# Kernel optimization log

Hardware: AMD Instinct MI355X
Metric: run time of the kernel (lower is better)

The kernel has to match this reference:

```python
import jax, jax.numpy as jnp
import numpy as np

N_DOF = 7
WIDTH = 1024
BATCH = 8192
EPS = 1e-5
LSIZE = N_DOF * (N_DOF + 1) // 2   # diag (n) + strictly-lower ((n^2-n)/2)


def _tri_idx(n):
    # order matches LowTri: offset -i chunks, within-chunk j -> entry (j+i, j)
    r, c = [], []
    for i in range(n):
        for j in range(n - i):
            r.append(j + i)
            c.append(j)
    return np.array(r, np.int32), np.array(c, np.int32)

_R, _C = _tri_idx(N_DOF)


def setup_inputs() -> dict:
    key = jax.random.key(0)
    ks = jax.random.split(key, 9)

    def glorot(k, shape):
        std = (2.0 / (shape[0] + shape[1])) ** 0.5
        return (jax.random.normal(k, shape, jnp.float32) * std).astype(jnp.float32)

    lower = LSIZE - N_DOF
    b0 = 0.1
    return {
        "state": jax.random.normal(ks[0], (BATCH, N_DOF), jnp.float32),
        "velocity": jax.random.normal(ks[1], (BATCH, N_DOF), jnp.float32),
        "acceleration": jax.random.normal(ks[2], (BATCH, N_DOF), jnp.float32),
        "W_in": glorot(ks[3], (N_DOF, WIDTH)), "b_in": jnp.full((WIDTH,), b0, jnp.float32),
        "W_h": glorot(ks[4], (WIDTH, WIDTH)), "b_h": jnp.full((WIDTH,), b0, jnp.float32),
        "W_g": glorot(ks[5], (WIDTH, 1)), "b_g": jnp.full((1,), b0, jnp.float32),
        "W_ld": glorot(ks[6], (WIDTH, N_DOF)), "b_ld": jnp.full((N_DOF,), b0, jnp.float32),
        "W_lo": glorot(ks[7], (WIDTH, lower)), "b_lo": jnp.full((lower,), b0, jnp.float32),
    }


def _layer(x, der, W, b, act):
    # a: [B, out]; der: [B, in, n_dof] -> [B, out, n_dof]
    a = x @ W + b
    if act == "relu":
        y = jax.nn.relu(a)
        gp = (a > 0).astype(a.dtype)
    else:  # linear
        y = a
        gp = jnp.ones_like(a)
    # diag(g'(a)) @ W^T @ prev_der  ==  g'(a)[:, :, None] * (W^T @ prev_der)
    new_der = gp[:, :, None] * jnp.einsum("io,bid->bod", W, der)
    return y, new_der


def _forward(state, velocity, acceleration,
             W_in, b_in, W_h, b_h, W_g, b_g, W_ld, b_ld, W_lo, b_lo):
    B = state.shape[0]
    eye = jnp.broadcast_to(jnp.eye(N_DOF, dtype=state.dtype), (B, N_DOF, N_DOF))

    y1, d1 = _layer(state, eye, W_in, b_in, "relu")
    y2, d2 = _layer(y1, d1, W_h, b_h, "relu")
    y3, d3 = _layer(y2, d2, W_h, b_h, "relu")   # original reuses hidden_layer1 twice

    V, derV = _layer(y3, d3, W_g, b_g, "linear")       # derV: [B, 1, n_dof]
    l_diag, der_ld = _layer(y3, d3, W_ld, b_ld, "relu")
    l_low, der_lo = _layer(y3, d3, W_lo, b_lo, "linear")

    l = jnp.concatenate([l_diag, l_low], axis=1)          # [B, LSIZE]
    der_l = jnp.concatenate([der_ld, der_lo], axis=1)     # [B, LSIZE, n_dof]

    def lowtri(v):   # [B, LSIZE] -> [B, n, n]
        return jnp.zeros((B, N_DOF, N_DOF), v.dtype).at[:, _R, _C].set(v)

    def lowtri3d(v):  # [B, n_dof, LSIZE] -> [B, n_dof, n, n]
        return jnp.zeros((B, N_DOF, N_DOF, N_DOF), v.dtype).at[:, :, _R, _C].set(v)

    L = lowtri(l)
    LT = jnp.swapaxes(L, 1, 2)
    M = L @ LT + EPS * jnp.eye(N_DOF, dtype=L.dtype)

    dldt = jnp.einsum("bld,bd->bl", der_l, velocity)
    dLdt = lowtri(dldt)
    dMdt = L @ jnp.swapaxes(dLdt, 1, 2) + dLdt @ LT

    dLdq = lowtri3d(jnp.swapaxes(der_l, 1, 2))            # [B, n_dof, n, n]
    dMdq = dLdq @ LT[:, None] + L[:, None] @ jnp.swapaxes(dLdq, 2, 3)

    dMdt_dq = jnp.einsum("bij,bj->bi", dMdt, velocity)
    quad_dq = jnp.einsum("bi,bkij,bj->bk", velocity, dMdq, velocity)
    C = dMdt_dq - 0.5 * quad_dq
    G = derV[:, 0, :]                                      # squeeze [B,1,n_dof]
    Mddq = jnp.einsum("bij,bj->bi", M, acceleration)
    tau_pred = Mddq + C + G
    return tau_pred, M, C, G


def reference(state, velocity, acceleration,
              W_in, b_in, W_h, b_h, W_g, b_g, W_ld, b_ld, W_lo, b_lo):
    return _forward(state, velocity, acceleration,
                    W_in, b_in, W_h, b_h, W_g, b_g, W_ld, b_ld, W_lo, b_lo)
```

## Files before the change

kernel.cpp:

```cpp
#include <hip/hip_runtime.h>
#include <hip/hip_bf16.h>

#define WIDTH 1024
#define BATCH 8192

typedef __attribute__((ext_vector_type(8))) short short8;
typedef __attribute__((ext_vector_type(4))) float floatx4;

typedef __attribute__((address_space(1))) void gvoid;
typedef __attribute__((address_space(3))) void lvoid;

__device__ __forceinline__ void async_copy16(const void* g, void* l) {
    __builtin_amdgcn_global_load_lds((gvoid*)g, (lvoid*)l, 16, 0, 0);
}

__device__ __forceinline__ void split_store(float v, __hip_bfloat16* hi, __hip_bfloat16* lo, long idx) {
    __hip_bfloat16 h = __float2bfloat16(v);
    hi[idx] = h;
    lo[idx] = __float2bfloat16(v - __bfloat162float(h));
}

template<int N> __device__ __forceinline__ void waitv() {
    if constexpr (N == 0)      asm volatile("s_waitcnt vmcnt(0)" ::: "memory");
    else if constexpr (N == 1) asm volatile("s_waitcnt vmcnt(1)" ::: "memory");
    else if constexpr (N == 3) asm volatile("s_waitcnt vmcnt(3)" ::: "memory");
    else if constexpr (N == 6) asm volatile("s_waitcnt vmcnt(6)" ::: "memory");
    else if constexpr (N == 7) asm volatile("s_waitcnt vmcnt(7)" ::: "memory");
    else if constexpr (N == 8) asm volatile("s_waitcnt vmcnt(8)" ::: "memory");
    else if constexpr (N == 9) asm volatile("s_waitcnt vmcnt(9)" ::: "memory");
}

__device__ __forceinline__ int swz_col(int s) {
    return ((s & 3) ^ ((s >> 3) & 3)) << 3;
}

__global__ __launch_bounds__(256) void transpose_k(
    const float* __restrict__ W,
    __hip_bfloat16* __restrict__ Wth, __hip_bfloat16* __restrict__ Wtl)
{
    __shared__ float t[32][33];
    const int tx = threadIdx.x & 31, ty = threadIdx.x >> 5;
    const int bx = blockIdx.x << 5, by = blockIdx.y << 5;
#pragma unroll
    for (int r = 0; r < 32; r += 8)
        t[ty + r][tx] = W[(long)(by + ty + r) * WIDTH + bx + tx];
    __syncthreads();
#pragma unroll
    for (int r = 0; r < 32; r += 8)
        split_store(t[tx][ty + r], Wth, Wtl, (long)(bx + ty + r) * WIDTH + by + tx);
}

__global__ __launch_bounds__(256) void buildwcat_k(
    const float* __restrict__ W_ld, const float* __restrict__ W_lo,
    const float* __restrict__ W_g,
    __hip_bfloat16* __restrict__ Wch, __hip_bfloat16* __restrict__ Wcl)
{
    const int idx = blockIdx.x * 256 + threadIdx.x;
    const int n = idx >> 10, k = idx & 1023;
    float v = 0.f;
    if (n < 7)       v = W_ld[k * 7 + n];
    else if (n < 28) v = W_lo[k * 21 + (n - 7)];
    else if (n == 28) v = W_g[k];
    split_store(v, Wch, Wcl, idx);
}

__global__ __launch_bounds__(256) void prep_k(
    const float* __restrict__ state,
    const float* __restrict__ W_in,
    const float* __restrict__ b_in,
    __hip_bfloat16* __restrict__ Y1h, __hip_bfloat16* __restrict__ Y1l,
    __hip_bfloat16* __restrict__ D1h)
{
    const int b = blockIdx.x;
    const int j0 = threadIdx.x * 4;
    float s[7];
#pragma unroll
    for (int d = 0; d < 7; ++d) s[d] = state[b * 7 + d];
    float a[4];
#pragma unroll
    for (int q = 0; q < 4; ++q) a[q] = b_in[j0 + q];
    float w[7][4];
#pragma unroll
    for (int d = 0; d < 7; ++d)
#pragma unroll
        for (int q = 0; q < 4; ++q) {
            w[d][q] = W_in[d * WIDTH + j0 + q];
            a[q] += s[d] * w[d][q];
        }
    bool gp[4];
#pragma unroll
    for (int q = 0; q < 4; ++q) {
        gp[q] = a[q] > 0.f;
        split_store(gp[q] ? a[q] : 0.f, Y1h, Y1l, (long)b * WIDTH + j0 + q);
    }
    union { unsigned long long u64; unsigned short h[4]; } pk;
#pragma unroll
    for (int d = 0; d < 7; ++d) {
#pragma unroll
        for (int q = 0; q < 4; ++q) {
            __hip_bfloat16 v = __float2bfloat16(gp[q] ? w[d][q] : 0.f);
            pk.h[q] = *reinterpret_cast<unsigned short*>(&v);
        }
        *reinterpret_cast<unsigned long long*>(&D1h[((long)b * 7 + d) * WIDTH + j0]) = pk.u64;
    }
}


__device__ __forceinline__ void st128(const short* src, short* region, int tid, int kbase) {
    async_copy16(src + (long)(tid >> 2) * WIDTH + kbase + swz_col(tid),
                 region + ((tid & 0x1C0) << 3));
}
__device__ __forceinline__ void st256(const short* src, short* region, int tid, int kbase) {
#pragma unroll
    for (int j = 0; j < 2; ++j) {
        const int idx = tid + (j << 9);
        async_copy16(src + (long)(idx >> 2) * WIDTH + kbase + swz_col(idx),
                     region + (((tid & 0x1C0) + (j << 9)) << 3));
    }
}

template<int W0, int W1, int W2, int IS>
__device__ __forceinline__ void y8_triple(
    short* buf, short* nbuf,
    const short* pAh, const short* pAl, const short* pBh, const short* pBl,
    int t, int tid, int wm, int wn, int r, int kqs, floatx4 (&acc)[4][4])
{
    short8 fah[4], fbh[4];
#pragma unroll
    for (int i = 0; i < 4; ++i)
        fah[i] = *reinterpret_cast<const short8*>(&buf[(wm * 64 + i * 16 + r) * 32 + kqs]);
#pragma unroll
    for (int j = 0; j < 4; ++j)
        fbh[j] = *reinterpret_cast<const short8*>(&buf[8192 + (wn * 64 + j * 16 + r) * 32 + kqs]);
    if (IS >= 1) st128(pAl, nbuf + 4096, tid, (t + 1) * 32);
    __builtin_amdgcn_s_barrier();
    asm volatile("s_waitcnt lgkmcnt(0)");
    __builtin_amdgcn_sched_barrier(0);
    __builtin_amdgcn_s_setprio(1);
#pragma unroll
    for (int i = 0; i < 4; ++i)
#pragma unroll
        for (int j = 0; j < 4; ++j)
            acc[i][j] = __builtin_amdgcn_mfma_f32_16x16x32_bf16(fah[i], fbh[j], acc[i][j], 0, 0, 0);
    __builtin_amdgcn_s_setprio(0);
    waitv<W0>();
    __builtin_amdgcn_s_barrier();
    short8 fbl[4];
#pragma unroll
    for (int j = 0; j < 4; ++j)
        fbl[j] = *reinterpret_cast<const short8*>(&buf[16384 + (wn * 64 + j * 16 + r) * 32 + kqs]);
    if (IS >= 2) { st128(pAh, buf, tid, (t + 2) * 32); st256(pBh, buf + 8192, tid, (t + 2) * 32); }
    __builtin_amdgcn_s_barrier();
    asm volatile("s_waitcnt lgkmcnt(0)");
    __builtin_amdgcn_sched_barrier(0);
    __builtin_amdgcn_s_setprio(1);
#pragma unroll
    for (int i = 0; i < 4; ++i)
#pragma unroll
        for (int j = 0; j < 4; ++j)
            acc[i][j] = __builtin_amdgcn_mfma_f32_16x16x32_bf16(fah[i], fbl[j], acc[i][j], 0, 0, 0);
    __builtin_amdgcn_s_setprio(0);
    waitv<W1>();
    __builtin_amdgcn_s_barrier();
    short8 fal[4];
#pragma unroll
    for (int i = 0; i < 4; ++i)
        fal[i] = *reinterpret_cast<const short8*>(&buf[4096 + (wm * 64 + i * 16 + r) * 32 + kqs]);
    if (IS >= 2) st256(pBl, buf + 16384, tid, (t + 2) * 32);
    __builtin_amdgcn_s_barrier();
    asm volatile("s_waitcnt lgkmcnt(0)");
    __builtin_amdgcn_sched_barrier(0);
    __builtin_amdgcn_s_setprio(1);
#pragma unroll
    for (int i = 0; i < 4; ++i)
#pragma unroll
        for (int j = 0; j < 4; ++j)
            acc[i][j] = __builtin_amdgcn_mfma_f32_16x16x32_bf16(fal[i], fbh[j], acc[i][j], 0, 0, 0);
    __builtin_amdgcn_s_setprio(0);
    waitv<W2>();
    __builtin_amdgcn_s_barrier();
}

__device__ __forceinline__ void y8_gemm_body(
    short* SM,
    int bm, int bn, int tid,
    const __hip_bfloat16* Ah_, const __hip_bfloat16* Al_,
    const __hip_bfloat16* Bh_, const __hip_bfloat16* Bl_,
    const float* bias,
    __hip_bfloat16* outh, __hip_bfloat16* outl)
{
    const int lane = tid & 63, wv = tid >> 6;
    const int wm = wv >> 2, wn = wv & 3;
    const int r = lane & 15, r4 = (lane >> 4) << 2;
    const int kqs = (((lane >> 4) ^ ((r >> 1) & 3)) << 3);
    const short* pAh = (const short*)Ah_ + (long)bm * 128 * WIDTH;
    const short* pAl = (const short*)Al_ + (long)bm * 128 * WIDTH;
    const short* pBh = (const short*)Bh_ + (long)bn * 256 * WIDTH;
    const short* pBl = (const short*)Bl_ + (long)bn * 256 * WIDTH;

    floatx4 acc[4][4] = {};

    st128(pAh, SM + 0,     tid, 0);
    st256(pBh, SM + 8192,  tid, 0);
    st256(pBl, SM + 16384, tid, 0);
    st128(pAl, SM + 4096,  tid, 0);
    st128(pAh, SM + 24576 + 0,     tid, 32);
    st256(pBh, SM + 24576 + 8192,  tid, 32);
    st256(pBl, SM + 24576 + 16384, tid, 32);
    waitv<8>();
    __builtin_amdgcn_s_barrier();

    for (int t2 = 0; t2 < 15; ++t2) {
        y8_triple<7, 9, 8, 2>(SM,         SM + 24576, pAh, pAl, pBh, pBl, 2 * t2,     tid, wm, wn, r, kqs, acc);
        y8_triple<7, 9, 8, 2>(SM + 24576, SM,         pAh, pAl, pBh, pBl, 2 * t2 + 1, tid, wm, wn, r, kqs, acc);
    }
    y8_triple<7, 6, 3, 1>(SM,         SM + 24576, pAh, pAl, pBh, pBl, 30, tid, wm, wn, r, kqs, acc);
    y8_triple<1, 0, 0, 0>(SM + 24576, SM,         pAh, pAl, pBh, pBl, 31, tid, wm, wn, r, kqs, acc);

#pragma unroll
    for (int i = 0; i < 4; ++i)
#pragma unroll
        for (int j = 0; j < 4; ++j) {
            const int col = bn * 256 + wn * 64 + j * 16 + r;
#pragma unroll
            for (int rr = 0; rr < 4; ++rr) {
                const int row = bm * 128 + wm * 64 + i * 16 + r4 + rr;
                float v = acc[i][j][rr] + bias[col];
                v = v > 0.f ? v : 0.f;
                split_store(v, outh, outl, (long)row * WIDTH + col);
            }
        }
}

__global__ __launch_bounds__(512, 2) void gemm_y8(
    const __hip_bfloat16* __restrict__ Ah, const __hip_bfloat16* __restrict__ Al,
    const __hip_bfloat16* __restrict__ Bh, const __hip_bfloat16* __restrict__ Bl,
    const float* __restrict__ bias,
    __hip_bfloat16* __restrict__ outh, __hip_bfloat16* __restrict__ outl)
{
    __shared__ __align__(16) short SM[49152];
    y8_gemm_body(SM, blockIdx.x, blockIdx.y, threadIdx.x, Ah, Al, Bh, Bl, bias, outh, outl);
}

__device__ __forceinline__ void stage_chunk_d2(
    short* SMbase, const short* __restrict__ A, const short* __restrict__ B,
    int tau, int c, int tid)
{
    const short* src = (c & 1) ? B : A;
    const int kbase = (tau << 6) + ((c >> 1) << 5);
    short* region = SMbase + ((tau & 1) << 15) + (c << 13);
    const int wvb = tid & 0x1C0;
#pragma unroll
    for (int j = 0; j < 2; ++j) {
        const int idx = tid + (j << 9);
        async_copy16(src + (long)(idx >> 2) * WIDTH + kbase + swz_col(idx),
                     region + ((long)(wvb + (j << 9)) << 3));
    }
}

__device__ __forceinline__ void d_gemm_256(
    short* SM, const short* Abase, const short* Bbase, int tid,
    int wm, int wn, int r, int kqs, floatx4 (&acc)[8][4])
{
    stage_chunk_d2(SM, Abase, Bbase, 0, 0, tid);
    stage_chunk_d2(SM, Abase, Bbase, 0, 1, tid);
    stage_chunk_d2(SM, Abase, Bbase, 0, 2, tid);
    stage_chunk_d2(SM, Abase, Bbase, 0, 3, tid);
    stage_chunk_d2(SM, Abase, Bbase, 1, 0, tid);
    stage_chunk_d2(SM, Abase, Bbase, 1, 1, tid);
    stage_chunk_d2(SM, Abase, Bbase, 1, 2, tid);
    asm volatile("s_waitcnt vmcnt(10)" ::: "memory");
    __builtin_amdgcn_s_barrier();

    short8 af[8], bf[2];
#pragma unroll 2
    for (int t = 0; t < 16; ++t) {
        short* buf = SM + ((t & 1) << 15);
#pragma unroll
        for (int ks = 0; ks < 2; ++ks) {
            const short* Ab = buf + (ks ? 2 : 0) * 8192;
            const short* Bb = buf + (ks ? 3 : 1) * 8192;

#pragma unroll
            for (int i = 0; i < 8; ++i)
                af[i] = *reinterpret_cast<const short8*>(&Ab[(wm * 128 + i * 16 + r) * 32 + kqs]);
#pragma unroll
            for (int j = 0; j < 2; ++j)
                bf[j] = *reinterpret_cast<const short8*>(&Bb[(wn * 64 + j * 16 + r) * 32 + kqs]);
            if (ks == 0) { if (t + 1 < 16) stage_chunk_d2(SM, Abase, Bbase, t + 1, 3, tid); }
            else         { if (t + 2 < 16) stage_chunk_d2(SM, Abase, Bbase, t + 2, 1, tid); }
            __builtin_amdgcn_s_barrier();
            asm volatile("s_waitcnt lgkmcnt(0)");
            __builtin_amdgcn_sched_barrier(0);
            __builtin_amdgcn_s_setprio(1);
#pragma unroll
            for (int i = 0; i < 8; ++i)
#pragma unroll
                for (int j = 0; j < 2; ++j)
                    acc[i][j] = __builtin_amdgcn_mfma_f32_16x16x32_bf16(af[i], bf[j], acc[i][j], 0, 0, 0);
            __builtin_amdgcn_s_setprio(0);
            __builtin_amdgcn_s_barrier();

#pragma unroll
            for (int j = 0; j < 2; ++j)
                bf[j] = *reinterpret_cast<const short8*>(&Bb[(wn * 64 + (2 + j) * 16 + r) * 32 + kqs]);
            if (ks == 0) { if (t + 2 < 16) stage_chunk_d2(SM, Abase, Bbase, t + 2, 0, tid); }
            else         { if (t + 2 < 16) stage_chunk_d2(SM, Abase, Bbase, t + 2, 2, tid); }
            __builtin_amdgcn_s_barrier();
            asm volatile("s_waitcnt lgkmcnt(0)");
            __builtin_amdgcn_sched_barrier(0);
            __builtin_amdgcn_s_setprio(1);
#pragma unroll
            for (int i = 0; i < 8; ++i)
#pragma unroll
                for (int j = 0; j < 2; ++j)
                    acc[i][2 + j] = __builtin_amdgcn_mfma_f32_16x16x32_bf16(af[i], bf[j], acc[i][2 + j], 0, 0, 0);
            __builtin_amdgcn_s_setprio(0);
            if (ks == 0) {
                if (t < 14)       asm volatile("s_waitcnt vmcnt(10)" ::: "memory");
                else if (t == 14) asm volatile("s_waitcnt vmcnt(8)"  ::: "memory");
                else              asm volatile("s_waitcnt vmcnt(0)"  ::: "memory");
            } else {
                if (t < 14)       asm volatile("s_waitcnt vmcnt(10)" ::: "memory");
                else if (t == 14) asm volatile("s_waitcnt vmcnt(4)"  ::: "memory");
            }
            __builtin_amdgcn_s_barrier();
        }
    }
}

__global__ __launch_bounds__(512, 2) void d2y3_8p(
    const __hip_bfloat16* __restrict__ D1,
    const __hip_bfloat16* __restrict__ Wth, const __hip_bfloat16* __restrict__ Wtl,
    const __hip_bfloat16* __restrict__ Y2h, const __hip_bfloat16* __restrict__ Y2l,
    const float* __restrict__ bias,
    __hip_bfloat16* __restrict__ D2out,
    __hip_bfloat16* __restrict__ Y3h, __hip_bfloat16* __restrict__ Y3l,
    int nd2)
{
    __shared__ __align__(16) short SM[65536];
    const int tid = threadIdx.x;

    if ((int)blockIdx.x >= nd2) {
        y8_gemm_body(SM, blockIdx.x - nd2, blockIdx.y, tid, Y2h, Y2l, Wth, Wtl, bias, Y3h, Y3l);
        return;
    }

    const short* Abase = (const short*)D1 + (long)blockIdx.x * 256 * WIDTH;
    const short* Bbase = (const short*)Wth + (long)blockIdx.y * 256 * WIDTH;
    const int lane = tid & 63, wv = tid >> 6;
    const int wm = wv >> 2, wn = wv & 3;
    const int r = lane & 15;
    const int kqs = (((lane >> 4) ^ ((r >> 1) & 3)) << 3);

    floatx4 acc[8][4] = {};
    d_gemm_256(SM, Abase, Bbase, tid, wm, wn, r, kqs, acc);

    const int r4 = (lane >> 4) << 2;
#pragma unroll
    for (int i = 0; i < 8; ++i)
#pragma unroll
        for (int j = 0; j < 4; ++j) {
            const int col = blockIdx.y * 256 + wn * 64 + j * 16 + r;
#pragma unroll
            for (int rr = 0; rr < 4; ++rr) {
                const int row = blockIdx.x * 256 + wm * 128 + i * 16 + r4 + rr;
                float v = acc[i][j][rr];
                const unsigned brow = (unsigned)row / 7u;
                if (!(__bfloat162float(Y2h[(long)brow * WIDTH + col]) > 0.f)) v = 0.f;
                D2out[(long)row * WIDTH + col] = __float2bfloat16(v);
            }
        }
}

__device__ __forceinline__ void heady_half(
    short* SMh, int bm, int tl,
    const __hip_bfloat16* __restrict__ Y3h, const __hip_bfloat16* __restrict__ Y3l,
    const __hip_bfloat16* __restrict__ Wch, const __hip_bfloat16* __restrict__ Wcl,
    float* __restrict__ PY)
{
    short* Ash = SMh;          short* Asl = SMh + 4096;
    short* Bsh = SMh + 8192;   short* Bsl = SMh + 9216;
    const int lane = tl & 63;
    const int wv = tl >> 6;
    const int r = lane & 15, r4 = (lane >> 4) << 2;
    const int kqs = (((lane >> 4) ^ ((r >> 1) & 3)) << 3);
    const int srow = tl >> 2, scol = (tl & 3) << 3;
    const int swc = (((tl & 3) ^ ((srow >> 1) & 3)) << 3);
    const long half = 64l * WIDTH;
    const short* pAh = (const short*)Y3h + (long)(bm * 128 + srow) * WIDTH + swc;
    const short* pAl = (const short*)Y3l + (long)(bm * 128 + srow) * WIDTH + swc;
    const long boff = (long)srow * WIDTH + scol;
    const short* pBh = (const short*)Wch;  const short* pBl = (const short*)Wcl;
// ... 12 lines not shown
        async_copy16(pAl + half + kt, Asl + 2048 + wv * 512);
        if (tl < 128) {
            *reinterpret_cast<short8*>(&Bsh[srow * 32 + swc]) = gbh;
            *reinterpret_cast<short8*>(&Bsl[srow * 32 + swc]) = gbl;
        }
        __syncthreads();
        short8 afh[2], afl[2], bfh[2], bfl[2];
#pragma unroll
        for (int i = 0; i < 2; ++i) {
            const int ar = (wv * 32 + i * 16 + r) * 32 + kqs;
            afh[i] = *reinterpret_cast<const short8*>(&Ash[ar]);
            afl[i] = *reinterpret_cast<const short8*>(&Asl[ar]);
        }
#pragma unroll
        for (int j = 0; j < 2; ++j) {
            const int br = (j * 16 + r) * 32 + kqs;
            bfh[j] = *reinterpret_cast<const short8*>(&Bsh[br]);
            bfl[j] = *reinterpret_cast<const short8*>(&Bsl[br]);
        }
#pragma unroll
        for (int i = 0; i < 2; ++i)
#pragma unroll
            for (int j = 0; j < 2; ++j) {
                acc[i][j] = __builtin_amdgcn_mfma_f32_16x16x32_bf16(afh[i], bfh[j], acc[i][j], 0, 0, 0);
                acc[i][j] = __builtin_amdgcn_mfma_f32_16x16x32_bf16(afh[i], bfl[j], acc[i][j], 0, 0, 0);
                acc[i][j] = __builtin_amdgcn_mfma_f32_16x16x32_bf16(afl[i], bfh[j], acc[i][j], 0, 0, 0);
            }
    }
#pragma unroll
    for (int i = 0; i < 2; ++i)
#pragma unroll
        for (int j = 0; j < 2; ++j)
#pragma unroll
            for (int rr = 0; rr < 4; ++rr) {
                const int row = bm * 128 + wv * 32 + i * 16 + r4 + rr;
                PY[(long)row * 32 + j * 16 + r] = acc[i][j][rr];
            }
}

__global__ __launch_bounds__(512, 2) void d3pd_8p(
    const __hip_bfloat16* __restrict__ D2,
    const __hip_bfloat16* __restrict__ Wth, const __hip_bfloat16* __restrict__ Wtl,
    const __hip_bfloat16* __restrict__ Y3h, const __hip_bfloat16* __restrict__ Y3l,
    const __hip_bfloat16* __restrict__ Wch, const __hip_bfloat16* __restrict__ Wcl,
    float* __restrict__ PDpart, float* __restrict__ PY,
    int nd2, int Mrows)
{
    __shared__ __align__(16) short SM[65536];
    const int tid = threadIdx.x;

    if ((int)blockIdx.x >= nd2) {
        if (blockIdx.y != 0) return;
        const int hd = (blockIdx.x - nd2) * 2 + (tid >> 8);
        heady_half(SM + (tid >> 8) * 10240, hd, tid & 255, Y3h, Y3l, Wch, Wcl, PY);
        return;
    }

    const int lane = tid & 63, wv = tid >> 6;
    const int wm = wv >> 2, wn = wv & 3;
    const int r = lane & 15, kq = (lane >> 4) << 3, r4 = (lane >> 4) << 2;
    const int kqs = (((lane >> 4) ^ ((r >> 1) & 3)) << 3);
    const int bm = blockIdx.x, bn = blockIdx.y;
    const short* Abase = (const short*)D2 + (long)bm * 256 * WIDTH;
    const short* Bbase = (const short*)Wth + (long)bn * 256 * WIDTH;

    floatx4 acc[8][4] = {};
    d_gemm_256(SM, Abase, Bbase, tid, wm, wn, r, kqs, acc);

    short* T   = SM;
    short* WcH = SM + 34816;
    short* WcL = SM + 39168;

    floatx4 accp[2][2] = {};
#pragma unroll
    for (int h = 0; h < 2; ++h) {
        __syncthreads();
        if ((wn >> 1) == h) {
#pragma unroll
            for (int i = 0; i < 8; ++i)
#pragma unroll
                for (int j = 0; j < 4; ++j) {
                    const int ct = (wn & 1) * 64 + j * 16 + r;
                    const int colg = bn * 256 + h * 128 + ct;
#pragma unroll
                    for (int rr = 0; rr < 4; ++rr) {
                        const int rowl = wm * 128 + i * 16 + r4 + rr;
                        const int rowg = bm * 256 + rowl;
                        float v = acc[i][j][rr];
                        const unsigned brow = (unsigned)rowg / 7u;
                        if (!(__bfloat162float(Y3h[(long)brow * WIDTH + colg]) > 0.f)) v = 0.f;
                        __hip_bfloat16 hb = __float2bfloat16(v);
                        T[rowl * 136 + ct] = *reinterpret_cast<short*>(&hb);
                    }
                }
        }
        {
            const int n = tid >> 4, k8 = (tid & 15) * 8;
            const short* wh = (const short*)Wch;
            const short* wl = (const short*)Wcl;
            *reinterpret_cast<short8*>(&WcH[n * 136 + k8]) =
                *reinterpret_cast<const short8*>(wh + (long)n * WIDTH + bn * 256 + h * 128 + k8);
            *reinterpret_cast<short8*>(&WcL[n * 136 + k8]) =
                *reinterpret_cast<const short8*>(wl + (long)n * WIDTH + bn * 256 + h * 128 + k8);
        }
        __syncthreads();
#pragma unroll
        for (int kk = 0; kk < 128; kk += 32) {
            short8 af2[2], bh8[2], bl8[2];
#pragma unroll
            for (int i = 0; i < 2; ++i)
                af2[i] = *reinterpret_cast<const short8*>(&T[(wv * 32 + i * 16 + r) * 136 + kk + kq]);
#pragma unroll
            for (int j = 0; j < 2; ++j) {
                bh8[j] = *reinterpret_cast<const short8*>(&WcH[(j * 16 + r) * 136 + kk + kq]);
                bl8[j] = *reinterpret_cast<const short8*>(&WcL[(j * 16 + r) * 136 + kk + kq]);
            }
#pragma unroll
            for (int i = 0; i < 2; ++i)
#pragma unroll
                for (int j = 0; j < 2; ++j) {
                    accp[i][j] = __builtin_amdgcn_mfma_f32_16x16x32_bf16(af2[i], bh8[j], accp[i][j], 0, 0, 0);
                    accp[i][j] = __builtin_amdgcn_mfma_f32_16x16x32_bf16(af2[i], bl8[j], accp[i][j], 0, 0, 0);
                }
        }
    }
#pragma unroll
    for (int i = 0; i < 2; ++i)
#pragma unroll
        for (int j = 0; j < 2; ++j)
#pragma unroll
            for (int rr = 0; rr < 4; ++rr) {
                const int rowg = bm * 256 + wv * 32 + i * 16 + r4 + rr;
                PDpart[((long)bn * Mrows + rowg) * 32 + j * 16 + r] = accp[i][j][rr];
            }
}

__device__ __forceinline__ int midx(int rr, int cc) {
    const int i = rr - cc;
    return i * 7 - (i * (i - 1)) / 2 + cc;
}

__global__ __launch_bounds__(64) void finalize_k(
    const float* __restrict__ PY,
    const float* __restrict__ PDpart,
    const float* __restrict__ vel_g,
    const float* __restrict__ acc_g,
// ... 87 lines not shown
        out[516096 + (long)b * 7 + tid] = Gv[tid];
    }
}

extern "C" void kernel_launch(void* const* d_in, const int* in_sizes, int n_in,
                              void* d_out, int out_size, void* d_ws, size_t ws_size,
                              hipStream_t stream)
{
    const float* state = (const float*)d_in[0];
    const float* vel   = (const float*)d_in[1];
    const float* accel = (const float*)d_in[2];
    const float* W_in  = (const float*)d_in[3];
    const float* b_in  = (const float*)d_in[4];
    const float* W_h   = (const float*)d_in[5];
    const float* b_h   = (const float*)d_in[6];
    const float* W_g   = (const float*)d_in[7];
    const float* W_ld  = (const float*)d_in[9];
    const float* b_ld  = (const float*)d_in[10];
    const float* W_lo  = (const float*)d_in[11];
    const float* b_lo  = (const float*)d_in[12];
    float* outp = (float*)d_out;

    char* ws = (char*)d_ws;
    __hip_bfloat16* Wth = (__hip_bfloat16*)ws; ws += (size_t)WIDTH * WIDTH * 2;
    __hip_bfloat16* Wtl = (__hip_bfloat16*)ws; ws += (size_t)WIDTH * WIDTH * 2;
    __hip_bfloat16* Wch = (__hip_bfloat16*)ws; ws += 32 * WIDTH * 2;
    __hip_bfloat16* Wcl = (__hip_bfloat16*)ws; ws += 32 * WIDTH * 2;
    const size_t fixed = (size_t)(ws - (char*)d_ws);

    int CH = 256;
    for (int cand = 8192; cand >= 256; cand >>= 1) {
        size_t need = fixed + (size_t)cand * 37120;
        if (need <= ws_size) { CH = cand; break; }
    }
    const int NCH = BATCH / CH;

    const size_t YB = (size_t)CH * WIDTH * 2;
    const size_t DB = (size_t)CH * 7 * WIDTH * 2;
    __hip_bfloat16* Yah = (__hip_bfloat16*)ws; ws += YB;
    __hip_bfloat16* Yal = (__hip_bfloat16*)ws; ws += YB;
    __hip_bfloat16* Ybh = (__hip_bfloat16*)ws; ws += YB;
    __hip_bfloat16* Ybl = (__hip_bfloat16*)ws; ws += YB;
    __hip_bfloat16* Dah = (__hip_bfloat16*)ws; ws += DB;
    __hip_bfloat16* Dbh = (__hip_bfloat16*)ws; ws += DB;
    float* PY = (float*)ws; ws += (size_t)CH * 32 * 4;
    float* PDpart = (float*)Dah;

    const int Mrows = CH * 7;
    const int nd2 = Mrows / 256;
    const int ny128 = CH / 128;

    transpose_k<<<dim3(32, 32), dim3(256), 0, stream>>>(W_h, Wth, Wtl);
    buildwcat_k<<<dim3(128), dim3(256), 0, stream>>>(W_ld, W_lo, W_g, Wch, Wcl);

    for (int c = 0; c < NCH; ++c) {
        prep_k<<<dim3(CH), dim3(256), 0, stream>>>(state + (size_t)c * CH * 7, W_in, b_in,
                                                   Yah, Yal, Dah);
        gemm_y8<<<dim3(ny128, 4), dim3(512), 0, stream>>>(
            Yah, Yal, Wth, Wtl, b_h, Ybh, Ybl);
        d2y3_8p<<<dim3(nd2 + ny128, 4), dim3(512), 0, stream>>>(
            Dah, Wth, Wtl, Ybh, Ybl, b_h, Dbh, Yah, Yal, nd2);
        d3pd_8p<<<dim3(nd2 + ny128 / 2, 4), dim3(512), 0, stream>>>(
            Dbh, Wth, Wtl, Yah, Yal, Wch, Wcl, PDpart, PY, nd2, Mrows);
        finalize_k<<<dim3(CH), dim3(64), 0, stream>>>(PY, PDpart, vel, accel, b_ld, b_lo,
                                                      outp, c * CH, Mrows);
    }
    (void)in_sizes; (void)n_in; (void)out_size;
}
```

Before: 577.8 us.

## Switch derivative GEMMs to fp16 and retile split-bf16 Y GEMM to 256x256

Derivative tensors and the transposed hidden weights are now stored as fp16 and multiplied with fp16 MFMA. The extra low-part bf16 correction products in the derivative paths and the output head are dropped, which cuts MFMA count and memory traffic. The split-bf16 Y GEMM is retiled from 128x256 to 256x256 with a reworked double-buffered staging pipeline, and grids are flattened to 1D. fp16 has a smaller range than bf16, so derivative values risk overflow or precision loss, and an extra fp16 weight copy is built.

```diff
diff --git a/kernel.cpp b/kernel.cpp
--- a/kernel.cpp
+++ b/kernel.cpp
@@ -1,10 +1,12 @@
 #include <hip/hip_runtime.h>
 #include <hip/hip_bf16.h>
+#include <hip/hip_fp16.h>
 
 #define WIDTH 1024
 #define BATCH 8192
 
 typedef __attribute__((ext_vector_type(8))) short short8;
+typedef __attribute__((ext_vector_type(8))) _Float16 half8;
 typedef __attribute__((ext_vector_type(4))) float floatx4;
 
 typedef __attribute__((address_space(1))) void gvoid;
@@ -20,14 +22,20 @@
     lo[idx] = __float2bfloat16(v - __bfloat162float(h));
 }
 
+__device__ __forceinline__ floatx4 mfma16(short8 a, short8 b, floatx4 c) {
+    return __builtin_amdgcn_mfma_f32_16x16x32_f16(
+        __builtin_bit_cast(half8, a), __builtin_bit_cast(half8, b), c, 0, 0, 0);
+}
+__device__ __forceinline__ floatx4 mfmabf(short8 a, short8 b, floatx4 c) {
+    return __builtin_amdgcn_mfma_f32_16x16x32_bf16(a, b, c, 0, 0, 0);
+}
+
 template<int N> __device__ __forceinline__ void waitv() {
     if constexpr (N == 0)      asm volatile("s_waitcnt vmcnt(0)" ::: "memory");
-    else if constexpr (N == 1) asm volatile("s_waitcnt vmcnt(1)" ::: "memory");
-    else if constexpr (N == 3) asm volatile("s_waitcnt vmcnt(3)" ::: "memory");
+    else if constexpr (N == 2) asm volatile("s_waitcnt vmcnt(2)" ::: "memory");
+    else if constexpr (N == 4) asm volatile("s_waitcnt vmcnt(4)" ::: "memory");
     else if constexpr (N == 6) asm volatile("s_waitcnt vmcnt(6)" ::: "memory");
-    else if constexpr (N == 7) asm volatile("s_waitcnt vmcnt(7)" ::: "memory");
     else if constexpr (N == 8) asm volatile("s_waitcnt vmcnt(8)" ::: "memory");
-    else if constexpr (N == 9) asm volatile("s_waitcnt vmcnt(9)" ::: "memory");
 }
 
 __device__ __forceinline__ int swz_col(int s) {
@@ -36,7 +44,8 @@
 
 __global__ __launch_bounds__(256) void transpose_k(
     const float* __restrict__ W,
-    __hip_bfloat16* __restrict__ Wth, __hip_bfloat16* __restrict__ Wtl)
+    __hip_bfloat16* __restrict__ Wthb, __hip_bfloat16* __restrict__ Wtlb,
+    __half* __restrict__ Wtf)
 {
     __shared__ float t[32][33];
     const int tx = threadIdx.x & 31, ty = threadIdx.x >> 5;
@@ -46,14 +55,19 @@
         t[ty + r][tx] = W[(long)(by + ty + r) * WIDTH + bx + tx];
     __syncthreads();
 #pragma unroll
-    for (int r = 0; r < 32; r += 8)
-        split_store(t[tx][ty + r], Wth, Wtl, (long)(bx + ty + r) * WIDTH + by + tx);
+    for (int r = 0; r < 32; r += 8) {
+        const float v = t[tx][ty + r];
+        const long idx = (long)(bx + ty + r) * WIDTH + by + tx;
+        split_store(v, Wthb, Wtlb, idx);
+        Wtf[idx] = __float2half(v);
+    }
 }
 
 __global__ __launch_bounds__(256) void buildwcat_k(
     const float* __restrict__ W_ld, const float* __restrict__ W_lo,
     const float* __restrict__ W_g,
-    __hip_bfloat16* __restrict__ Wch, __hip_bfloat16* __restrict__ Wcl)
+    __hip_bfloat16* __restrict__ Wchb, __hip_bfloat16* __restrict__ Wclb,
+    __half* __restrict__ Wcf)
 {
     const int idx = blockIdx.x * 256 + threadIdx.x;
     const int n = idx >> 10, k = idx & 1023;
@@ -61,7 +75,8 @@
     if (n < 7)       v = W_ld[k * 7 + n];
     else if (n < 28) v = W_lo[k * 21 + (n - 7)];
     else if (n == 28) v = W_g[k];
-    split_store(v, Wch, Wcl, idx);
+    split_store(v, Wchb, Wclb, idx);
+    Wcf[idx] = __float2half(v);
 }
 
 __global__ __launch_bounds__(256) void prep_k(
@@ -69,7 +84,7 @@
     const float* __restrict__ W_in,
     const float* __restrict__ b_in,
     __hip_bfloat16* __restrict__ Y1h, __hip_bfloat16* __restrict__ Y1l,
-    __hip_bfloat16* __restrict__ D1h)
+    __half* __restrict__ D1f)
 {
     const int b = blockIdx.x;
     const int j0 = threadIdx.x * 4;
@@ -98,148 +113,103 @@
     for (int d = 0; d < 7; ++d) {
 #pragma unroll
         for (int q = 0; q < 4; ++q) {
-            __hip_bfloat16 v = __float2bfloat16(gp[q] ? w[d][q] : 0.f);
+            __half v = __float2half(gp[q] ? w[d][q] : 0.f);
             pk.h[q] = *reinterpret_cast<unsigned short*>(&v);
         }
-        *reinterpret_cast<unsigned long long*>(&D1h[((long)b * 7 + d) * WIDTH + j0]) = pk.u64;
-    }
-}
-
-
-__device__ __forceinline__ void st128(const short* src, short* region, int tid, int kbase) {
-    async_copy16(src + (long)(tid >> 2) * WIDTH + kbase + swz_col(tid),
-                 region + ((tid & 0x1C0) << 3));
-}
-__device__ __forceinline__ void st256(const short* src, short* region, int tid, int kbase) {
+        *reinterpret_cast<unsigned long long*>(&D1f[((long)b * 7 + d) * WIDTH + j0]) = pk.u64;
+    }
+}
+
+__device__ __forceinline__ void stage_s(
+    short* SMbase, const short* __restrict__ src, int tau, int reg, int tid)
+{
+    short* region = SMbase + ((tau & 1) << 15) + (reg << 13);
+    const int wvb = tid & 0x1C0;
+    const int kt = tau << 5;
 #pragma unroll
     for (int j = 0; j < 2; ++j) {
         const int idx = tid + (j << 9);
-        async_copy16(src + (long)(idx >> 2) * WIDTH + kbase + swz_col(idx),
-                     region + (((tid & 0x1C0) + (j << 9)) << 3));
+        async_copy16(src + (long)(idx >> 2) * WIDTH + kt + swz_col(idx),
+                     region + ((long)(wvb + (j << 9)) << 3));
     }
 }
 
 template<int W0, int W1, int W2, int IS>
-__device__ __forceinline__ void y8_triple(
-    short* buf, short* nbuf,
-    const short* pAh, const short* pAl, const short* pBh, const short* pBl,
-    int t, int tid, int wm, int wn, int r, int kqs, floatx4 (&acc)[4][4])
-{
-    short8 fah[4], fbh[4];
-#pragma unroll
-    for (int i = 0; i < 4; ++i)
-        fah[i] = *reinterpret_cast<const short8*>(&buf[(wm * 64 + i * 16 + r) * 32 + kqs]);
+__device__ __forceinline__ void ys_step(
+    short* SM, const short* pAh, const short* pAl, const short* pBh, const short* pBl,
+    int t, int tid, int wm, int wn, int r, int kqs, floatx4 (&acc)[8][4])
+{
+    short* buf = SM + ((t & 1) << 15);
+    short8 ah[8], bh[4];
+#pragma unroll
+    for (int i = 0; i < 8; ++i)
+        ah[i] = *reinterpret_cast<const short8*>(&buf[(wm * 128 + i * 16 + r) * 32 + kqs]);
 #pragma unroll
     for (int j = 0; j < 4; ++j)
-        fbh[j] = *reinterpret_cast<const short8*>(&buf[8192 + (wn * 64 + j * 16 + r) * 32 + kqs]);
-    if (IS >= 1) st128(pAl, nbuf + 4096, tid, (t + 1) * 32);
+        bh[j] = *reinterpret_cast<const short8*>(&buf[8192 + (wn * 64 + j * 16 + r) * 32 + kqs]);
+    if (IS) { stage_s(SM, pAh, t + 1, 0, tid); stage_s(SM, pBh, t + 1, 1, tid); }
     __builtin_amdgcn_s_barrier();
     asm volatile("s_waitcnt lgkmcnt(0)");
     __builtin_amdgcn_sched_barrier(0);
     __builtin_amdgcn_s_setprio(1);
 #pragma unroll
-    for (int i = 0; i < 4; ++i)
+    for (int i = 0; i < 8; ++i)
 #pragma unroll
         for (int j = 0; j < 4; ++j)
-            acc[i][j] = __builtin_amdgcn_mfma_f32_16x16x32_bf16(fah[i], fbh[j], acc[i][j], 0, 0, 0);
+            acc[i][j] = mfmabf(ah[i], bh[j], acc[i][j]);
     __builtin_amdgcn_s_setprio(0);
     waitv<W0>();
     __builtin_amdgcn_s_barrier();
-    short8 fbl[4];
-#pragma unroll
-    for (int j = 0; j < 4; ++j)
-        fbl[j] = *reinterpret_cast<const short8*>(&buf[16384 + (wn * 64 + j * 16 + r) * 32 + kqs]);
-    if (IS >= 2) { st128(pAh, buf, tid, (t + 2) * 32); st256(pBh, buf + 8192, tid, (t + 2) * 32); }
+    short8 al[8];
+#pragma unroll
+    for (int i = 0; i < 8; ++i)
+        al[i] = *reinterpret_cast<const short8*>(&buf[16384 + (wm * 128 + i * 16 + r) * 32 + kqs]);
+    if (IS) stage_s(SM, pAl, t + 1, 2, tid);
     __builtin_amdgcn_s_barrier();
     asm volatile("s_waitcnt lgkmcnt(0)");
     __builtin_amdgcn_sched_barrier(0);
     __builtin_amdgcn_s_setprio(1);
 #pragma unroll
-    for (int i = 0; i < 4; ++i)
+    for (int i = 0; i < 8; ++i)
 #pragma unroll
         for (int j = 0; j < 4; ++j)
-            acc[i][j] = __builtin_amdgcn_mfma_f32_16x16x32_bf16(fah[i], fbl[j], acc[i][j], 0, 0, 0);
+            acc[i][j] = mfmabf(al[i], bh[j], acc[i][j]);
     __builtin_amdgcn_s_setprio(0);
     waitv<W1>();
     __builtin_amdgcn_s_barrier();
-    short8 fal[4];
-#pragma unroll
-    for (int i = 0; i < 4; ++i)
-        fal[i] = *reinterpret_cast<const short8*>(&buf[4096 + (wm * 64 + i * 16 + r) * 32 + kqs]);
-    if (IS >= 2) st256(pBl, buf + 16384, tid, (t + 2) * 32);
+    short8 bl[4];
+#pragma unroll
+    for (int j = 0; j < 4; ++j)
+        bl[j] = *reinterpret_cast<const short8*>(&buf[24576 + (wn * 64 + j * 16 + r) * 32 + kqs]);
+    if (IS) stage_s(SM, pBl, t + 1, 3, tid);
     __builtin_amdgcn_s_barrier();
     asm volatile("s_waitcnt lgkmcnt(0)");
     __builtin_amdgcn_sched_barrier(0);
     __builtin_amdgcn_s_setprio(1);
 #pragma unroll
-    for (int i = 0; i < 4; ++i)
+    for (int i = 0; i < 8; ++i)
 #pragma unroll
         for (int j = 0; j < 4; ++j)
-            acc[i][j] = __builtin_amdgcn_mfma_f32_16x16x32_bf16(fal[i], fbh[j], acc[i][j], 0, 0, 0);
+            acc[i][j] = mfmabf(ah[i], bl[j], acc[i][j]);
     __builtin_amdgcn_s_setprio(0);
     waitv<W2>();
     __builtin_amdgcn_s_barrier();
 }
 
-__device__ __forceinline__ void y8_gemm_body(
-    short* SM,
-    int bm, int bn, int tid,
-    const __hip_bfloat16* Ah_, const __hip_bfloat16* Al_,
-    const __hip_bfloat16* Bh_, const __hip_bfloat16* Bl_,
-    const float* bias,
-    __hip_bfloat16* outh, __hip_bfloat16* outl)
-{
-    const int lane = tid & 63, wv = tid >> 6;
-    const int wm = wv >> 2, wn = wv & 3;
-    const int r = lane & 15, r4 = (lane >> 4) << 2;
-    const int kqs = (((lane >> 4) ^ ((r >> 1) & 3)) << 3);
-    const short* pAh = (const short*)Ah_ + (long)bm * 128 * WIDTH;
-    const short* pAl = (const short*)Al_ + (long)bm * 128 * WIDTH;
-    const short* pBh = (const short*)Bh_ + (long)bn * 256 * WIDTH;
-    const short* pBl = (const short*)Bl_ + (long)bn * 256 * WIDTH;
-
-    floatx4 acc[4][4] = {};
-
-    st128(pAh, SM + 0,     tid, 0);
-    st256(pBh, SM + 8192,  tid, 0);
-    st256(pBl, SM + 16384, tid, 0);
-    st128(pAl, SM + 4096,  tid, 0);
-    st128(pAh, SM + 24576 + 0,     tid, 32);
-    st256(pBh, SM + 24576 + 8192,  tid, 32);
-    st256(pBl, SM + 24576 + 16384, tid, 32);
-    waitv<8>();
+__device__ __forceinline__ void ys_gemm_256(
+    short* SM, const short* Ah, const short* Al, const short* Bh, const short* Bl,
+    int tid, int wm, int wn, int r, int kqs, floatx4 (&acc)[8][4])
+{
+    stage_s(SM, Ah, 0, 0, tid);
+    stage_s(SM, Bh, 0, 1, tid);
+    stage_s(SM, Al, 0, 2, tid);
+    stage_s(SM, Bl, 0, 3, tid);
+    waitv<4>();
     __builtin_amdgcn_s_barrier();
-
-    for (int t2 = 0; t2 < 15; ++t2) {
-        y8_triple<7, 9, 8, 2>(SM,         SM + 24576, pAh, pAl, pBh, pBl, 2 * t2,     tid, wm, wn, r, kqs, acc);
-        y8_triple<7, 9, 8, 2>(SM + 24576, SM,         pAh, pAl, pBh, pBl, 2 * t2 + 1, tid, wm, wn, r, kqs, acc);
-    }
-    y8_triple<7, 6, 3, 1>(SM,         SM + 24576, pAh, pAl, pBh, pBl, 30, tid, wm, wn, r, kqs, acc);
-    y8_triple<1, 0, 0, 0>(SM + 24576, SM,         pAh, pAl, pBh, pBl, 31, tid, wm, wn, r, kqs, acc);
-
-#pragma unroll
-    for (int i = 0; i < 4; ++i)
-#pragma unroll
-        for (int j = 0; j < 4; ++j) {
-            const int col = bn * 256 + wn * 64 + j * 16 + r;
-#pragma unroll
-            for (int rr = 0; rr < 4; ++rr) {
-                const int row = bm * 128 + wm * 64 + i * 16 + r4 + rr;
-                float v = acc[i][j][rr] + bias[col];
-                v = v > 0.f ? v : 0.f;
-                split_store(v, outh, outl, (long)row * WIDTH + col);
-            }
-        }
-}
-
-__global__ __launch_bounds__(512, 2) void gemm_y8(
-    const __hip_bfloat16* __restrict__ Ah, const __hip_bfloat16* __restrict__ Al,
-    const __hip_bfloat16* __restrict__ Bh, const __hip_bfloat16* __restrict__ Bl,
-    const float* __restrict__ bias,
-    __hip_bfloat16* __restrict__ outh, __hip_bfloat16* __restrict__ outl)
-{
-    __shared__ __align__(16) short SM[49152];
-    y8_gemm_body(SM, blockIdx.x, blockIdx.y, threadIdx.x, Ah, Al, Bh, Bl, bias, outh, outl);
+#pragma unroll 2
+    for (int t = 0; t < 31; ++t)
+        ys_step<6, 6, 4, 1>(SM, Ah, Al, Bh, Bl, t, tid, wm, wn, r, kqs, acc);
+    ys_step<2, 0, 99, 0>(SM, Ah, Al, Bh, Bl, 31, tid, wm, wn, r, kqs, acc);
 }
 
 __device__ __forceinline__ void stage_chunk_d2(
@@ -268,11 +238,10 @@
     stage_chunk_d2(SM, Abase, Bbase, 0, 3, tid);
     stage_chunk_d2(SM, Abase, Bbase, 1, 0, tid);
     stage_chunk_d2(SM, Abase, Bbase, 1, 1, tid);
-    stage_chunk_d2(SM, Abase, Bbase, 1, 2, tid);
-    asm volatile("s_waitcnt vmcnt(10)" ::: "memory");
+    waitv<8>();
     __builtin_amdgcn_s_barrier();
 
-    short8 af[8], bf[2];
+    short8 af[8], bf[4];
 #pragma unroll 2
     for (int t = 0; t < 16; ++t) {
         short* buf = SM + ((t & 1) << 15);
@@ -282,11 +251,28 @@
             const short* Bb = buf + (ks ? 3 : 1) * 8192;
 
 #pragma unroll
-            for (int i = 0; i < 8; ++i)
+            for (int i = 0; i < 4; ++i)
                 af[i] = *reinterpret_cast<const short8*>(&Ab[(wm * 128 + i * 16 + r) * 32 + kqs]);
 #pragma unroll
-            for (int j = 0; j < 2; ++j)
+            for (int j = 0; j < 4; ++j)
                 bf[j] = *reinterpret_cast<const short8*>(&Bb[(wn * 64 + j * 16 + r) * 32 + kqs]);
+            if (ks == 0) { if (t + 1 < 16) stage_chunk_d2(SM, Abase, Bbase, t + 1, 2, tid); }
+            else         { if (t + 2 < 16) stage_chunk_d2(SM, Abase, Bbase, t + 2, 0, tid); }
+            __builtin_amdgcn_s_barrier();
+            asm volatile("s_waitcnt lgkmcnt(0)");
+            __builtin_amdgcn_sched_barrier(0);
+            __builtin_amdgcn_s_setprio(1);
+#pragma unroll
+            for (int i = 0; i < 4; ++i)
+#pragma unroll
+                for (int j = 0; j < 4; ++j)
+                    acc[i][j] = mfma16(af[i], bf[j], acc[i][j]);
+            __builtin_amdgcn_s_setprio(0);
+            __builtin_amdgcn_s_barrier();
+
+#pragma unroll
+            for (int i = 0; i < 4; ++i)
+                af[4 + i] = *reinterpret_cast<const short8*>(&Ab[(wm * 128 + (4 + i) * 16 + r) * 32 + kqs]);
             if (ks == 0) { if (t + 1 < 16) stage_chunk_d2(SM, Abase, Bbase, t + 1, 3, tid); }
             else         { if (t + 2 < 16) stage_chunk_d2(SM, Abase, Bbase, t + 2, 1, tid); }
             __builtin_amdgcn_s_barrier();
@@ -294,81 +280,107 @@
             __builtin_amdgcn_sched_barrier(0);
             __builtin_amdgcn_s_setprio(1);
 #pragma unroll
-            for (int i = 0; i < 8; ++i)
-#pragma unroll
-                for (int j = 0; j < 2; ++j)
-                    acc[i][j] = __builtin_amdgcn_mfma_f32_16x16x32_bf16(af[i], bf[j], acc[i][j], 0, 0, 0);
-            __builtin_amdgcn_s_setprio(0);
-            __builtin_amdgcn_s_barrier();
-
-#pragma unroll
-            for (int j = 0; j < 2; ++j)
-                bf[j] = *reinterpret_cast<const short8*>(&Bb[(wn * 64 + (2 + j) * 16 + r) * 32 + kqs]);
-            if (ks == 0) { if (t + 2 < 16) stage_chunk_d2(SM, Abase, Bbase, t + 2, 0, tid); }
-            else         { if (t + 2 < 16) stage_chunk_d2(SM, Abase, Bbase, t + 2, 2, tid); }
-            __builtin_amdgcn_s_barrier();
-            asm volatile("s_waitcnt lgkmcnt(0)");
-            __builtin_amdgcn_sched_barrier(0);
-            __builtin_amdgcn_s_setprio(1);
-#pragma unroll
-            for (int i = 0; i < 8; ++i)
-#pragma unroll
-                for (int j = 0; j < 2; ++j)
-                    acc[i][2 + j] = __builtin_amdgcn_mfma_f32_16x16x32_bf16(af[i], bf[j], acc[i][2 + j], 0, 0, 0);
+            for (int i = 0; i < 4; ++i)
+#pragma unroll
+                for (int j = 0; j < 4; ++j)
+                    acc[4 + i][j] = mfma16(af[4 + i], bf[j], acc[4 + i][j]);
             __builtin_amdgcn_s_setprio(0);
             if (ks == 0) {
-                if (t < 14)       asm volatile("s_waitcnt vmcnt(10)" ::: "memory");
-                else if (t == 14) asm volatile("s_waitcnt vmcnt(8)"  ::: "memory");
-                else              asm volatile("s_waitcnt vmcnt(0)"  ::: "memory");
+                if (t < 15) waitv<8>(); else waitv<0>();
             } else {
-                if (t < 14)       asm volatile("s_waitcnt vmcnt(10)" ::: "memory");
-                else if (t == 14) asm volatile("s_waitcnt vmcnt(4)"  ::: "memory");
+                if (t < 14) waitv<8>(); else if (t == 14) waitv<4>();
             }
             __builtin_amdgcn_s_barrier();
         }
     }
 }
 
+__device__ __forceinline__ void y_epilogue_s(
+    floatx4 (&acc)[8][4], const float* __restrict__ bias,
+    __hip_bfloat16* __restrict__ outh, __hip_bfloat16* __restrict__ outl,
+    int bx, int by, int wm, int wn, int r, int r4)
+{
+#pragma unroll
+    for (int i = 0; i < 8; ++i)
+#pragma unroll
+        for (int j = 0; j < 4; ++j) {
+            const int col = by * 256 + wn * 64 + j * 16 + r;
+#pragma unroll
+            for (int rr = 0; rr < 4; ++rr) {
+                const int row = bx * 256 + wm * 128 + i * 16 + r4 + rr;
+                float v = acc[i][j][rr] + bias[col];
+                v = v > 0.f ? v : 0.f;
+                split_store(v, outh, outl, (long)row * WIDTH + col);
+            }
+        }
+}
+
+__global__ __launch_bounds__(512, 2) void gemm_ys(
+    const __hip_bfloat16* __restrict__ Ah, const __hip_bfloat16* __restrict__ Al,
+    const __hip_bfloat16* __restrict__ Bh, const __hip_bfloat16* __restrict__ Bl,
+    const float* __restrict__ bias,
+    __hip_bfloat16* __restrict__ outh, __hip_bfloat16* __restrict__ outl)
+{
+    __shared__ __align__(16) short SM[65536];
+    const int tid = threadIdx.x;
+    const int lane = tid & 63, wv = tid >> 6;
+    const int wm = wv >> 2, wn = wv & 3;
+    const int r = lane & 15, r4 = (lane >> 4) << 2;
+    const int kqs = (((lane >> 4) ^ ((r >> 1) & 3)) << 3);
+    const int bm = blockIdx.x >> 2, bn = blockIdx.x & 3;
+    floatx4 acc[8][4] = {};
+    ys_gemm_256(SM, (const short*)Ah + (long)bm * 256 * WIDTH,
+                (const short*)Al + (long)bm * 256 * WIDTH,
+                (const short*)Bh + (long)bn * 256 * WIDTH,
+                (const short*)Bl + (long)bn * 256 * WIDTH, tid, wm, wn, r, kqs, acc);
+    y_epilogue_s(acc, bias, outh, outl, bm, bn, wm, wn, r, r4);
+}
+
 __global__ __launch_bounds__(512, 2) void d2y3_8p(
-    const __hip_bfloat16* __restrict__ D1,
-    const __hip_bfloat16* __restrict__ Wth, const __hip_bfloat16* __restrict__ Wtl,
+    const __half* __restrict__ D1,
+    const __half* __restrict__ Wtf,
+    const __hip_bfloat16* __restrict__ Wthb, const __hip_bfloat16* __restrict__ Wtlb,
     const __hip_bfloat16* __restrict__ Y2h, const __hip_bfloat16* __restrict__ Y2l,
     const float* __restrict__ bias,
-    __hip_bfloat16* __restrict__ D2out,
+    __half* __restrict__ D2out,
     __hip_bfloat16* __restrict__ Y3h, __hip_bfloat16* __restrict__ Y3l,
-    int nd2)
+    int ny)
 {
     __shared__ __align__(16) short SM[65536];
     const int tid = threadIdx.x;
-
-    if ((int)blockIdx.x >= nd2) {
-        y8_gemm_body(SM, blockIdx.x - nd2, blockIdx.y, tid, Y2h, Y2l, Wth, Wtl, bias, Y3h, Y3l);
-        return;
-    }
-
-    const short* Abase = (const short*)D1 + (long)blockIdx.x * 256 * WIDTH;
-    const short* Bbase = (const short*)Wth + (long)blockIdx.y * 256 * WIDTH;
     const int lane = tid & 63, wv = tid >> 6;
     const int wm = wv >> 2, wn = wv & 3;
-    const int r = lane & 15;
+    const int r = lane & 15, r4 = (lane >> 4) << 2;
     const int kqs = (((lane >> 4) ^ ((r >> 1) & 3)) << 3);
 
     floatx4 acc[8][4] = {};
-    d_gemm_256(SM, Abase, Bbase, tid, wm, wn, r, kqs, acc);
-
-    const int r4 = (lane >> 4) << 2;
+    if ((int)blockIdx.x < ny * 4) {
+        const int bm = blockIdx.x >> 2, bn = blockIdx.x & 3;
+        ys_gemm_256(SM, (const short*)Y2h + (long)bm * 256 * WIDTH,
+                    (const short*)Y2l + (long)bm * 256 * WIDTH,
+                    (const short*)Wthb + (long)bn * 256 * WIDTH,
+                    (const short*)Wtlb + (long)bn * 256 * WIDTH, tid, wm, wn, r, kqs, acc);
+        y_epilogue_s(acc, bias, Y3h, Y3l, bm, bn, wm, wn, r, r4);
+        return;
+    }
+
+    const int d = blockIdx.x - ny * 4;
+    const int bm = d >> 2, bn = d & 3;
+    d_gemm_256(SM, (const short*)D1 + (long)bm * 256 * WIDTH,
+               (const short*)Wtf + (long)bn * 256 * WIDTH, tid, wm, wn, r, kqs, acc);
+
 #pragma unroll
     for (int i = 0; i < 8; ++i)
 #pragma unroll
         for (int j = 0; j < 4; ++j) {
-            const int col = blockIdx.y * 256 + wn * 64 + j * 16 + r;
+            const int col = bn * 256 + wn * 64 + j * 16 + r;
 #pragma unroll
             for (int rr = 0; rr < 4; ++rr) {
-                const int row = blockIdx.x * 256 + wm * 128 + i * 16 + r4 + rr;
+                const int row = bm * 256 + wm * 128 + i * 16 + r4 + rr;
                 float v = acc[i][j][rr];
                 const unsigned brow = (unsigned)row / 7u;
                 if (!(__bfloat162float(Y2h[(long)brow * WIDTH + col]) > 0.f)) v = 0.f;
-                D2out[(long)row * WIDTH + col] = __float2bfloat16(v);
+                D2out[(long)row * WIDTH + col] = __float2half(v);
             }
         }
 }
@@ -427,9 +439,9 @@
         for (int i = 0; i < 2; ++i)
 #pragma unroll
             for (int j = 0; j < 2; ++j) {
-                acc[i][j] = __builtin_amdgcn_mfma_f32_16x16x32_bf16(afh[i], bfh[j], acc[i][j], 0, 0, 0);
-                acc[i][j] = __builtin_amdgcn_mfma_f32_16x16x32_bf16(afh[i], bfl[j], acc[i][j], 0, 0, 0);
-                acc[i][j] = __builtin_amdgcn_mfma_f32_16x16x32_bf16(afl[i], bfh[j], acc[i][j], 0, 0, 0);
+                acc[i][j] = mfmabf(afh[i], bfh[j], acc[i][j]);
+                acc[i][j] = mfmabf(afh[i], bfl[j], acc[i][j]);
+                acc[i][j] = mfmabf(afl[i], bfh[j], acc[i][j]);
             }
     }
 #pragma unroll
@@ -444,20 +456,20 @@
 }
 
 __global__ __launch_bounds__(512, 2) void d3pd_8p(
-    const __hip_bfloat16* __restrict__ D2,
-    const __hip_bfloat16* __restrict__ Wth, const __hip_bfloat16* __restrict__ Wtl,
+    const __half* __restrict__ D2,
+    const __half* __restrict__ Wtf,
     const __hip_bfloat16* __restrict__ Y3h, const __hip_bfloat16* __restrict__ Y3l,
-    const __hip_bfloat16* __restrict__ Wch, const __hip_bfloat16* __restrict__ Wcl,
+    const __half* __restrict__ Wcf,
+    const __hip_bfloat16* __restrict__ Wchb, const __hip_bfloat16* __restrict__ Wclb,
     float* __restrict__ PDpart, float* __restrict__ PY,
     int nd2, int Mrows)
 {
     __shared__ __align__(16) short SM[65536];
     const int tid = threadIdx.x;
 
-    if ((int)blockIdx.x >= nd2) {
-        if (blockIdx.y != 0) return;
-        const int hd = (blockIdx.x - nd2) * 2 + (tid >> 8);
-        heady_half(SM + (tid >> 8) * 10240, hd, tid & 255, Y3h, Y3l, Wch, Wcl, PY);
+    if ((int)blockIdx.x >= nd2 * 4) {
+        const int hd = (blockIdx.x - nd2 * 4) * 2 + (tid >> 8);
+        heady_half(SM + (tid >> 8) * 10240, hd, tid & 255, Y3h, Y3l, Wchb, Wclb, PY);
         return;
     }
 
@@ -465,16 +477,14 @@
     const int wm = wv >> 2, wn = wv & 3;
     const int r = lane & 15, kq = (lane >> 4) << 3, r4 = (lane >> 4) << 2;
     const int kqs = (((lane >> 4) ^ ((r >> 1) & 3)) << 3);
-    const int bm = blockIdx.x, bn = blockIdx.y;
-    const short* Abase = (const short*)D2 + (long)bm * 256 * WIDTH;
-    const short* Bbase = (const short*)Wth + (long)bn * 256 * WIDTH;
+    const int bm = blockIdx.x >> 2, bn = blockIdx.x & 3;
 
     floatx4 acc[8][4] = {};
-    d_gemm_256(SM, Abase, Bbase, tid, wm, wn, r, kqs, acc);
+    d_gemm_256(SM, (const short*)D2 + (long)bm * 256 * WIDTH,
+               (const short*)Wtf + (long)bn * 256 * WIDTH, tid, wm, wn, r, kqs, acc);
 
     short* T   = SM;
     short* WcH = SM + 34816;
-    short* WcL = SM + 39168;
 
     floatx4 accp[2][2] = {};
 #pragma unroll
@@ -494,39 +504,32 @@
                         float v = acc[i][j][rr];
                         const unsigned brow = (unsigned)rowg / 7u;
                         if (!(__bfloat162float(Y3h[(long)brow * WIDTH + colg]) > 0.f)) v = 0.f;
-                        __hip_bfloat16 hb = __float2bfloat16(v);
+                        __half hb = __float2half(v);
                         T[rowl * 136 + ct] = *reinterpret_cast<short*>(&hb);
                     }
                 }
         }
         {
             const int n = tid >> 4, k8 = (tid & 15) * 8;
-            const short* wh = (const short*)Wch;
-            const short* wl = (const short*)Wcl;
+            const short* wh = (const short*)Wcf;
             *reinterpret_cast<short8*>(&WcH[n * 136 + k8]) =
                 *reinterpret_cast<const short8*>(wh + (long)n * WIDTH + bn * 256 + h * 128 + k8);
-            *reinterpret_cast<short8*>(&WcL[n * 136 + k8]) =
-                *reinterpret_cast<const short8*>(wl + (long)n * WIDTH + bn * 256 + h * 128 + k8);
         }
         __syncthreads();
 #pragma unroll
         for (int kk = 0; kk < 128; kk += 32) {
-            short8 af2[2], bh8[2], bl8[2];
+            short8 af2[2], bh8[2];
 #pragma unroll
             for (int i = 0; i < 2; ++i)
                 af2[i] = *reinterpret_cast<const short8*>(&T[(wv * 32 + i * 16 + r) * 136 + kk + kq]);
 #pragma unroll
-            for (int j = 0; j < 2; ++j) {
+            for (int j = 0; j < 2; ++j)
                 bh8[j] = *reinterpret_cast<const short8*>(&WcH[(j * 16 + r) * 136 + kk + kq]);
-                bl8[j] = *reinterpret_cast<const short8*>(&WcL[(j * 16 + r) * 136 + kk + kq]);
-            }
 #pragma unroll
             for (int i = 0; i < 2; ++i)
 #pragma unroll
-                for (int j = 0; j < 2; ++j) {
-                    accp[i][j] = __builtin_amdgcn_mfma_f32_16x16x32_bf16(af2[i], bh8[j], accp[i][j], 0, 0, 0);
-                    accp[i][j] = __builtin_amdgcn_mfma_f32_16x16x32_bf16(af2[i], bl8[j], accp[i][j], 0, 0, 0);
-                }
+                for (int j = 0; j < 2; ++j)
+                    accp[i][j] = mfma16(af2[i], bh8[j], accp[i][j]);
         }
     }
 #pragma unroll
@@ -660,15 +663,17 @@
     float* outp = (float*)d_out;
 
     char* ws = (char*)d_ws;
-    __hip_bfloat16* Wth = (__hip_bfloat16*)ws; ws += (size_t)WIDTH * WIDTH * 2;
-    __hip_bfloat16* Wtl = (__hip_bfloat16*)ws; ws += (size_t)WIDTH * WIDTH * 2;
-    __hip_bfloat16* Wch = (__hip_bfloat16*)ws; ws += 32 * WIDTH * 2;
-    __hip_bfloat16* Wcl = (__hip_bfloat16*)ws; ws += 32 * WIDTH * 2;
+    __hip_bfloat16* Wthb = (__hip_bfloat16*)ws; ws += (size_t)WIDTH * WIDTH * 2;
+    __hip_bfloat16* Wtlb = (__hip_bfloat16*)ws; ws += (size_t)WIDTH * WIDTH * 2;
+    __half*         Wtf  = (__half*)ws;         ws += (size_t)WIDTH * WIDTH * 2;
+    __hip_bfloat16* Wchb = (__hip_bfloat16*)ws; ws += 32 * WIDTH * 2;
+    __hip_bfloat16* Wclb = (__hip_bfloat16*)ws; ws += 32 * WIDTH * 2;
+    __half*         Wcf  = (__half*)ws;         ws += 32 * WIDTH * 2;
     const size_t fixed = (size_t)(ws - (char*)d_ws);
 
     int CH = 256;
     for (int cand = 8192; cand >= 256; cand >>= 1) {
-        size_t need = fixed + (size_t)cand * 37120;
+        size_t need = fixed + (size_t)cand * 36992;
         if (need <= ws_size) { CH = cand; break; }
     }
     const int NCH = BATCH / CH;
@@ -679,27 +684,27 @@
     __hip_bfloat16* Yal = (__hip_bfloat16*)ws; ws += YB;
     __hip_bfloat16* Ybh = (__hip_bfloat16*)ws; ws += YB;
     __hip_bfloat16* Ybl = (__hip_bfloat16*)ws; ws += YB;
-    __hip_bfloat16* Dah = (__hip_bfloat16*)ws; ws += DB;
-    __hip_bfloat16* Dbh = (__hip_bfloat16*)ws; ws += DB;
+    __half* Daf = (__half*)ws; ws += DB;
+    __half* Dbf = (__half*)ws; ws += DB;
     float* PY = (float*)ws; ws += (size_t)CH * 32 * 4;
-    float* PDpart = (float*)Dah;
+    float* PDpart = (float*)Daf;
 
     const int Mrows = CH * 7;
     const int nd2 = Mrows / 256;
-    const int ny128 = CH / 128;
-
-    transpose_k<<<dim3(32, 32), dim3(256), 0, stream>>>(W_h, Wth, Wtl);
-    buildwcat_k<<<dim3(128), dim3(256), 0, stream>>>(W_ld, W_lo, W_g, Wch, Wcl);
+    const int ny256 = CH / 256;
+
+    transpose_k<<<dim3(32, 32), dim3(256), 0, stream>>>(W_h, Wthb, Wtlb, Wtf);
+    buildwcat_k<<<dim3(128), dim3(256), 0, stream>>>(W_ld, W_lo, W_g, Wchb, Wclb, Wcf);
 
     for (int c = 0; c < NCH; ++c) {
         prep_k<<<dim3(CH), dim3(256), 0, stream>>>(state + (size_t)c * CH * 7, W_in, b_in,
-                                                   Yah, Yal, Dah);
-        gemm_y8<<<dim3(ny128, 4), dim3(512), 0, stream>>>(
-            Yah, Yal, Wth, Wtl, b_h, Ybh, Ybl);
-        d2y3_8p<<<dim3(nd2 + ny128, 4), dim3(512), 0, stream>>>(
-            Dah, Wth, Wtl, Ybh, Ybl, b_h, Dbh, Yah, Yal, nd2);
-        d3pd_8p<<<dim3(nd2 + ny128 / 2, 4), dim3(512), 0, stream>>>(
-            Dbh, Wth, Wtl, Yah, Yal, Wch, Wcl, PDpart, PY, nd2, Mrows);
+                                                   Yah, Yal, Daf);
+        gemm_ys<<<dim3(ny256 * 4), dim3(512), 0, stream>>>(
+            Yah, Yal, Wthb, Wtlb, b_h, Ybh, Ybl);
+        d2y3_8p<<<dim3((ny256 + nd2) * 4), dim3(512), 0, stream>>>(
+            Daf, Wtf, Wthb, Wtlb, Ybh, Ybl, b_h, Dbf, Yah, Yal, ny256);
+        d3pd_8p<<<dim3(nd2 * 4 + ny256), dim3(512), 0, stream>>>(
+            Dbf, Wtf, Yah, Yal, Wcf, Wchb, Wclb, PDpart, PY, nd2, Mrows);
         finalize_k<<<dim3(CH), dim3(64), 0, stream>>>(PY, PDpart, vel, accel, b_ld, b_lo,
                                                       outp, c * CH, Mrows);
     }
```

New measurement: 656.9 us. 13.7% more time.
